# Kernel optimization log

Hardware: AMD Instinct MI355X
Metric: run time of the kernel (lower is better)

## Reference

```python
import jax, jax.numpy as jnp
import numpy as np

# Static config (from set_param of the wrapped deformable conv)
N, CIN, H, W = 8, 64, 128, 128
COUT, KH, KW = 64, 3, 3
STRIDE, PAD, DIL = 1, 1, 1
WEIGHT_BIT = 8
K = KH * KW
HO = (H + 2 * PAD - DIL * (KH - 1) - 1) // STRIDE + 1
WO = (W + 2 * PAD - DIL * (KW - 1) - 1) // STRIDE + 1


def setup_inputs() -> dict:
    key = jax.random.key(0)
    k1, k2, k3 = jax.random.split(key, 3)
    x = jax.random.normal(k1, (N, CIN, H, W), dtype=jnp.float32)
    offset = jax.random.normal(k2, (N, 2 * K, HO, WO), dtype=jnp.float32)
    weight = jax.random.normal(k3, (COUT, CIN, KH, KW), dtype=jnp.float32) * 0.05
    return {"x": x, "offset": offset, "weight": weight}


def quantize_weight_symmetric(w, bits):
    # HAWQ/CoDeNet symmetric per-tensor quant: scale = max(|min|,|max|)/n,
    # q = clamp(round(w/scale), -n-1, n) * scale, straight-through estimator.
    n = 2 ** (bits - 1) - 1
    sat = jnp.maximum(jnp.abs(w.min()), jnp.abs(w.max()))
    scale = jnp.maximum(sat, 1e-8) / n
    wq = jnp.clip(jnp.round(w / scale), -n - 1, n) * scale
    return w + jax.lax.stop_gradient(wq - w)


def deform_conv2d(x, offset, weight):
    # x: [N,C,H,W]; offset: [N, 2*K, HO, WO] (y,x interleaved per kernel tap)
    # Base sampling grid for each kernel tap and output location.
    ky, kx = jnp.meshgrid(jnp.arange(KH), jnp.arange(KW), indexing='ij')
    ky = ky.reshape(K).astype(jnp.float32)  # [K]
    kx = kx.reshape(K).astype(jnp.float32)
    ho = jnp.arange(HO, dtype=jnp.float32)
    wo = jnp.arange(WO, dtype=jnp.float32)
    base_y = ho[None, :, None] * STRIDE - PAD + ky[:, None, None] * DIL  # [K,HO,1]
    base_x = wo[None, None, :] * STRIDE - PAD + kx[:, None, None] * DIL  # [K,1,WO]

    off = offset.reshape(N, K, 2, HO, WO)
    py = base_y[None] + off[:, :, 0]  # [N,K,HO,WO]
    px = base_x[None] + off[:, :, 1]

    y0 = jnp.floor(py)
    x0 = jnp.floor(px)
    dy = py - y0
    dx = px - x0
    y0i = y0.astype(jnp.int32)
    x0i = x0.astype(jnp.int32)

    xf = x.reshape(N, CIN, H * W)

    def gather_corner(yi, xi, wgt):
        # zero padding outside the image
        valid = (yi >= 0) & (yi < H) & (xi >= 0) & (xi < W)
        idx = jnp.clip(yi, 0, H - 1) * W + jnp.clip(xi, 0, W - 1)  # [N,K,HO,WO]
        vals = jax.vmap(lambda xn, idn: xn[:, idn.reshape(-1)])(xf, idx)
        vals = vals.reshape(N, CIN, K, HO, WO)
        return vals * (wgt * valid.astype(wgt.dtype))[:, None]  # [N,1,K,HO,WO]

    sampled = (
        gather_corner(y0i, x0i, (1.0 - dy) * (1.0 - dx))
        + gather_corner(y0i, x0i + 1, (1.0 - dy) * dx)
        + gather_corner(y0i + 1, x0i, dy * (1.0 - dx))
        + gather_corner(y0i + 1, x0i + 1, dy * dx)
    )  # [N,CIN,K,HO,WO]

    out = jnp.einsum('nckhw,ock->nohw', sampled, weight.reshape(COUT, CIN, K))
    return out


def reference(x, offset, weight):
    wq = quantize_weight_symmetric(weight, WEIGHT_BIT)
    return deform_conv2d(x, offset, wq)
```

## Files before the change

kernel.cpp:

```cpp
#include <hip/hip_runtime.h>
#include <hip/hip_bf16.h>

#define NB    8
#define CCH   64
#define HH    128
#define WW    128
#define KTAP  9
#define HW    (HH * WW)
#define KDIM  (CCH * KTAP)
#define KSTEPS 18
#define LDA   72

typedef __attribute__((ext_vector_type(8))) short bf16x8;
typedef __attribute__((ext_vector_type(4))) float f32x4;

__device__ inline unsigned int pack_bf16(float a, float b) {
    unsigned int ua = __float_as_uint(a);
    unsigned int ub = __float_as_uint(b);
    ua += 0x7fffu + ((ua >> 16) & 1u);
    ub += 0x7fffu + ((ub >> 16) & 1u);
    return (ua >> 16) | (ub & 0xffff0000u);
}

__device__ inline void cvt8(uint4 u, float* f) {
    f[0] = __uint_as_float(u.x << 16); f[1] = __uint_as_float(u.x & 0xffff0000u);
    f[2] = __uint_as_float(u.y << 16); f[3] = __uint_as_float(u.y & 0xffff0000u);
    f[4] = __uint_as_float(u.z << 16); f[5] = __uint_as_float(u.z & 0xffff0000u);
    f[6] = __uint_as_float(u.w << 16); f[7] = __uint_as_float(u.w & 0xffff0000u);
}

__global__ __launch_bounds__(256) void maxabs_kernel(const float* __restrict__ w,
                                                     unsigned int* __restrict__ out) {
    unsigned int m = 0;
    int i = blockIdx.x * 1024 + threadIdx.x;
    #pragma unroll
    for (int r = 0; r < 4; r++) {
        m = max(m, __float_as_uint(w[i]) & 0x7fffffffu);
        i += 256;
    }
    #pragma unroll
    for (int off = 32; off > 0; off >>= 1)
        m = max(m, (unsigned int)__shfl_down(m, off));
    if ((threadIdx.x & 63) == 0) atomicMax(out, m);
}

__global__ __launch_bounds__(256) void quant_frag_kernel(const float* __restrict__ w,
                                                         const unsigned int* __restrict__ maxabs_u,
                                                         uint4* __restrict__ bq) {
    int t = blockIdx.x * 256 + threadIdx.x;
    if (t >= 4608) return;
    float m = __uint_as_float(maxabs_u[0]);
    float scale = fmaxf(m, 1e-8f) / 127.f;
    int nt  = t / (KSTEPS * 64);
    int rem = t - nt * (KSTEPS * 64);
    int s    = rem >> 6;
    int lane = rem & 63;
    int quad = lane >> 4, n16 = lane & 15;
    int o = nt * 16 + n16;
    unsigned int u[4];
    #pragma unroll
    for (int jj = 0; jj < 4; jj++) {
        float q[2];
        #pragma unroll
        for (int h = 0; h < 2; h++) {
            int k   = s * 32 + quad * 8 + 2 * jj + h;
            int c   = k & 63;
            int tap = k >> 6;
            float v  = w[(o * CCH + c) * KTAP + tap];
            float qq = rintf(v / scale);
            q[h] = fminf(fmaxf(qq, -128.f), 127.f) * scale;
        }
        u[jj] = pack_bf16(q[0], q[1]);
    }
    bq[t] = make_uint4(u[0], u[1], u[2], u[3]);
}

__global__ __launch_bounds__(256) void transpose_kernel(const float* __restrict__ x,
                                                        unsigned int* __restrict__ xt32) {
    __shared__ float tile[64][65];
    const int t = threadIdx.x;
    const int n = blockIdx.x >> 8;
    const int pbase = (blockIdx.x & 255) * 64;
    #pragma unroll
    for (int i = 0; i < 16; i++) {
        int idx = i * 256 + t;
        int c = idx >> 6, pp = idx & 63;
        tile[c][pp] = x[((size_t)(n * CCH + c)) * HW + pbase + pp];
    }
    __syncthreads();
    #pragma unroll
    for (int j = 0; j < 8; j++) {
        int idx = j * 256 + t;
        int pp = idx >> 5, cp = idx & 31;
        xt32[((size_t)(n * HW + pbase + pp)) * 32 + cp] =
            pack_bf16(tile[2 * cp][pp], tile[2 * cp + 1][pp]);
    }
}

__global__ __launch_bounds__(256) void deform_mfma(const unsigned short* __restrict__ xt,
                                                   const float* __restrict__ offset,
                                                   const uint4* __restrict__ bq,
                                                   float* __restrict__ out) {
    __shared__ unsigned short Abuf[2][64 * LDA];

    const int t    = threadIdx.x;
    const int wid  = t >> 6;
    const int lane = t & 63;
    const int quad = lane >> 4, n16 = lane & 15;
    const int bid  = blockIdx.x;
    const int n    = bid & 7;
    const int px0  = (bid >> 3) * 64;
    const int p_local = t >> 2;
    const int cq      = (t & 3) * 16;
    const int ppx = px0 + p_local;
    const int ho  = ppx >> 7, wo = ppx & 127;

    const unsigned short* xtn = xt + (size_t)n * HW * CCH;
    const float* offn = offset + (size_t)n * 2 * KTAP * HW;

    uint4 bfrag[KSTEPS];
    #pragma unroll
    for (int s = 0; s < KSTEPS; s++)
        bfrag[s] = bq[(wid * KSTEPS + s) * 64 + lane];

    f32x4 acc[4];
    #pragma unroll
    for (int mt = 0; mt < 4; mt++) acc[mt] = (f32x4){0.f, 0.f, 0.f, 0.f};

    auto build = [&](int tap, int buf) {
        const int ky = tap / 3;
        const int kx = tap - 3 * ky;
        const float offy = offn[(2 * tap) * HW + ppx];
        const float offx = offn[(2 * tap + 1) * HW + ppx];
        const float py  = (float)(ho - 1 + ky) + offy;
        const float pxf = (float)(wo - 1 + kx) + offx;
        const float fy = floorf(py), fx = floorf(pxf);
        const int y0 = (int)fy, x0 = (int)fx;
        const float dy = py - fy, dx = pxf - fx;
        const int y1 = y0 + 1, x1 = x0 + 1;
        const bool vy0 = (y0 >= 0) && (y0 < HH);
        const bool vy1 = (y1 >= 0) && (y1 < HH);
        const bool vx0 = (x0 >= 0) && (x0 < WW);
        const bool vx1 = (x1 >= 0) && (x1 < WW);
        const int y0c = min(max(y0, 0), HH - 1);
        const int y1c = min(max(y1, 0), HH - 1);
        const int x0c = min(max(x0, 0), WW - 1);
        const int x1c = min(max(x1, 0), WW - 1);
        const float w00 = (1.f - dy) * (1.f - dx) * ((vy0 && vx0) ? 1.f : 0.f);
        const float w01 = (1.f - dy) * dx         * ((vy0 && vx1) ? 1.f : 0.f);
        const float w10 = dy * (1.f - dx)         * ((vy1 && vx0) ? 1.f : 0.f);
        const float w11 = dy * dx                 * ((vy1 && vx1) ? 1.f : 0.f);

        const unsigned short* p00 = xtn + (y0c * WW + x0c) * CCH + cq;
        const unsigned short* p01 = xtn + (y0c * WW + x1c) * CCH + cq;
        const unsigned short* p10 = xtn + (y1c * WW + x0c) * CCH + cq;
        const unsigned short* p11 = xtn + (y1c * WW + x1c) * CCH + cq;
        uint4 a00 = *(const uint4*)p00, b00 = *(const uint4*)(p00 + 8);
        uint4 a01 = *(const uint4*)p01, b01 = *(const uint4*)(p01 + 8);
        uint4 a10 = *(const uint4*)p10, b10 = *(const uint4*)(p10 + 8);
        uint4 a11 = *(const uint4*)p11, b11 = *(const uint4*)(p11 + 8);

        float s[16], f[16];
        cvt8(a00, f); cvt8(b00, f + 8);
        #pragma unroll
        for (int i = 0; i < 16; i++) s[i] = f[i] * w00;
        cvt8(a01, f); cvt8(b01, f + 8);
        #pragma unroll
        for (int i = 0; i < 16; i++) s[i] = fmaf(f[i], w01, s[i]);
        cvt8(a10, f); cvt8(b10, f + 8);
        #pragma unroll
        for (int i = 0; i < 16; i++) s[i] = fmaf(f[i], w10, s[i]);
        cvt8(a11, f); cvt8(b11, f + 8);
        #pragma unroll
        for (int i = 0; i < 16; i++) s[i] = fmaf(f[i], w11, s[i]);

        unsigned int o8[8];
        #pragma unroll
        for (int i = 0; i < 8; i++) o8[i] = pack_bf16(s[2 * i], s[2 * i + 1]);
        unsigned short* dst = &Abuf[buf][p_local * LDA + cq];
        *(uint4*)dst       = make_uint4(o8[0], o8[1], o8[2], o8[3]);
        *(uint4*)(dst + 8) = make_uint4(o8[4], o8[5], o8[6], o8[7]);
    };

    auto mma_tap = [&](int tap, int buf) {
        #pragma unroll
        for (int sl = 0; sl < 2; sl++) {
            const int sg = tap * 2 + sl;
            bf16x8 b = *(bf16x8*)&bfrag[sg];
            #pragma unroll
            for (int mt = 0; mt < 4; mt++) {
                const unsigned short* src =
                    &Abuf[buf][(mt * 16 + n16) * LDA + sl * 32 + quad * 8];
                bf16x8 a = *(const bf16x8*)src;
                acc[mt] = __builtin_amdgcn_mfma_f32_16x16x32_bf16(a, b, acc[mt], 0, 0, 0);
            }
        }
    };

    build(0, 0);
    __syncthreads();
    for (int tap = 0; tap < KTAP; tap++) {
        if (tap < KTAP - 1) build(tap + 1, (tap + 1) & 1);
        mma_tap(tap, tap & 1);
        __syncthreads();
    }

    const int o = wid * 16 + n16;
    #pragma unroll
    for (int mt = 0; mt < 4; mt++) {
        float4 v = make_float4(acc[mt].x, acc[mt].y, acc[mt].z, acc[mt].w);
        float* dst = out + ((size_t)(n * CCH + o)) * HW + px0 + mt * 16 + quad * 4;
        *(float4*)dst = v;
    }
}

extern "C" void kernel_launch(void* const* d_in, const int* in_sizes, int n_in,
                              void* d_out, int out_size, void* d_ws, size_t ws_size,
                              hipStream_t stream) {
    const float* x      = (const float*)d_in[0];
    const float* offset = (const float*)d_in[1];
    const float* weight = (const float*)d_in[2];
    float* out = (float*)d_out;

    unsigned char* ws = (unsigned char*)d_ws;
    unsigned int* maxabs_u = (unsigned int*)ws;
    uint4*        bq       = (uint4*)(ws + 1024);
    unsigned int* xt32     = (unsigned int*)(ws + 131072);
    unsigned short* xt     = (unsigned short*)xt32;

    hipMemsetAsync(maxabs_u, 0, 4, stream);
    maxabs_kernel<<<36, 256, 0, stream>>>(weight, maxabs_u);
    quant_frag_kernel<<<18, 256, 0, stream>>>(weight, maxabs_u, bq);
    transpose_kernel<<<NB * (HW / 64), 256, 0, stream>>>(x, xt32);
    deform_mfma<<<NB * (HW / 64), 256, 0, stream>>>(xt, offset, bq, out);
}
```

Baseline: 145.3 us.

## Fuse prep kernels, switch to fp16 packed math, precompute sampling indices in LDS

Merges the weight max-abs, quantize and transpose steps into a single prep kernel, which removes the memset and two extra launches. The main kernel now works in fp16 instead of bf16: bilinear interpolation uses packed half-precision vector math and the tensor op is the fp16 MFMA. Each block first computes all per-tap sampling offsets and weights into shared memory. The A tile uses an XOR swizzle instead of padding to avoid LDS bank conflicts. fp16 accumulation of the interpolation lowers precision and could overflow for large inputs.

```diff
diff --git a/kernel.cpp b/kernel.cpp
--- a/kernel.cpp
+++ b/kernel.cpp
@@ -7,93 +7,86 @@
 #define WW    128
 #define KTAP  9
 #define HW    (HH * WW)
-#define KDIM  (CCH * KTAP)
 #define KSTEPS 18
-#define LDA   72
-
-typedef __attribute__((ext_vector_type(8))) short bf16x8;
+
+typedef _Float16 f16x8 __attribute__((ext_vector_type(8)));
+typedef _Float16 f16x2 __attribute__((ext_vector_type(2)));
 typedef __attribute__((ext_vector_type(4))) float f32x4;
 
-__device__ inline unsigned int pack_bf16(float a, float b) {
-    unsigned int ua = __float_as_uint(a);
-    unsigned int ub = __float_as_uint(b);
-    ua += 0x7fffu + ((ua >> 16) & 1u);
-    ub += 0x7fffu + ((ub >> 16) & 1u);
-    return (ua >> 16) | (ub & 0xffff0000u);
-}
-
-__device__ inline void cvt8(uint4 u, float* f) {
-    f[0] = __uint_as_float(u.x << 16); f[1] = __uint_as_float(u.x & 0xffff0000u);
-    f[2] = __uint_as_float(u.y << 16); f[3] = __uint_as_float(u.y & 0xffff0000u);
-    f[4] = __uint_as_float(u.z << 16); f[5] = __uint_as_float(u.z & 0xffff0000u);
-    f[6] = __uint_as_float(u.w << 16); f[7] = __uint_as_float(u.w & 0xffff0000u);
-}
-
-__global__ __launch_bounds__(256) void maxabs_kernel(const float* __restrict__ w,
-                                                     unsigned int* __restrict__ out) {
-    unsigned int m = 0;
-    int i = blockIdx.x * 1024 + threadIdx.x;
-    #pragma unroll
-    for (int r = 0; r < 4; r++) {
-        m = max(m, __float_as_uint(w[i]) & 0x7fffffffu);
-        i += 256;
-    }
-    #pragma unroll
-    for (int off = 32; off > 0; off >>= 1)
-        m = max(m, (unsigned int)__shfl_down(m, off));
-    if ((threadIdx.x & 63) == 0) atomicMax(out, m);
-}
-
-__global__ __launch_bounds__(256) void quant_frag_kernel(const float* __restrict__ w,
-                                                         const unsigned int* __restrict__ maxabs_u,
-                                                         uint4* __restrict__ bq) {
-    int t = blockIdx.x * 256 + threadIdx.x;
-    if (t >= 4608) return;
-    float m = __uint_as_float(maxabs_u[0]);
-    float scale = fmaxf(m, 1e-8f) / 127.f;
-    int nt  = t / (KSTEPS * 64);
-    int rem = t - nt * (KSTEPS * 64);
-    int s    = rem >> 6;
-    int lane = rem & 63;
-    int quad = lane >> 4, n16 = lane & 15;
-    int o = nt * 16 + n16;
-    unsigned int u[4];
-    #pragma unroll
-    for (int jj = 0; jj < 4; jj++) {
-        float q[2];
-        #pragma unroll
-        for (int h = 0; h < 2; h++) {
-            int k   = s * 32 + quad * 8 + 2 * jj + h;
-            int c   = k & 63;
-            int tap = k >> 6;
-            float v  = w[(o * CCH + c) * KTAP + tap];
-            float qq = rintf(v / scale);
-            q[h] = fminf(fmaxf(qq, -128.f), 127.f) * scale;
+__device__ inline unsigned int pack_f16(float a, float b) {
+    f16x2 h;
+    h[0] = (_Float16)a;
+    h[1] = (_Float16)b;
+    return __builtin_bit_cast(unsigned int, h);
+}
+
+__global__ __launch_bounds__(256) void prep_kernel(const float* __restrict__ x,
+                                                   const float* __restrict__ w,
+                                                   unsigned int* __restrict__ xt32,
+                                                   uint4* __restrict__ bq) {
+    __shared__ float tile[64 * 65];
+    const int t = threadIdx.x;
+    const int bid = blockIdx.x;
+
+    if (bid < 2048) {
+        const int n = bid >> 8;
+        const int pbase = (bid & 255) * 64;
+        #pragma unroll
+        for (int i = 0; i < 4; i++) {
+            int idx = i * 256 + t;
+            int c = idx >> 4, f4 = idx & 15;
+            float4 v = *(const float4*)&x[((size_t)(n * CCH + c)) * HW + pbase + f4 * 4];
+            float* d = &tile[c * 65 + f4 * 4];
+            d[0] = v.x; d[1] = v.y; d[2] = v.z; d[3] = v.w;
         }
-        u[jj] = pack_bf16(q[0], q[1]);
-    }
-    bq[t] = make_uint4(u[0], u[1], u[2], u[3]);
-}
-
-__global__ __launch_bounds__(256) void transpose_kernel(const float* __restrict__ x,
-                                                        unsigned int* __restrict__ xt32) {
-    __shared__ float tile[64][65];
-    const int t = threadIdx.x;
-    const int n = blockIdx.x >> 8;
-    const int pbase = (blockIdx.x & 255) * 64;
-    #pragma unroll
-    for (int i = 0; i < 16; i++) {
-        int idx = i * 256 + t;
-        int c = idx >> 6, pp = idx & 63;
-        tile[c][pp] = x[((size_t)(n * CCH + c)) * HW + pbase + pp];
-    }
-    __syncthreads();
-    #pragma unroll
-    for (int j = 0; j < 8; j++) {
-        int idx = j * 256 + t;
-        int pp = idx >> 5, cp = idx & 31;
-        xt32[((size_t)(n * HW + pbase + pp)) * 32 + cp] =
-            pack_bf16(tile[2 * cp][pp], tile[2 * cp + 1][pp]);
+        __syncthreads();
+        const int px = t >> 2, c4 = t & 3;
+        float f[16];
+        #pragma unroll
+        for (int j = 0; j < 16; j++) f[j] = tile[(c4 * 16 + j) * 65 + px];
+        unsigned int o8[8];
+        #pragma unroll
+        for (int i = 0; i < 8; i++) o8[i] = pack_f16(f[2 * i], f[2 * i + 1]);
+        uint4* dst = (uint4*)&xt32[((size_t)(n * HW + pbase + px)) * 32 + c4 * 8];
+        dst[0] = make_uint4(o8[0], o8[1], o8[2], o8[3]);
+        dst[1] = make_uint4(o8[4], o8[5], o8[6], o8[7]);
+    } else {
+        float m = 0.f;
+        for (int i = t; i < CCH * CCH * KTAP; i += 256)
+            m = fmaxf(m, fabsf(w[i]));
+        #pragma unroll
+        for (int off = 32; off > 0; off >>= 1)
+            m = fmaxf(m, __shfl_down(m, off));
+        if ((t & 63) == 0) tile[t >> 6] = m;
+        __syncthreads();
+        m = fmaxf(fmaxf(tile[0], tile[1]), fmaxf(tile[2], tile[3]));
+        const float scale = fmaxf(m, 1e-8f) / 127.f;
+        const float inv_scale = 1.f / scale;
+
+        for (int rec = t; rec < 4608; rec += 256) {
+            int nt  = rec / (KSTEPS * 64);
+            int rem = rec - nt * (KSTEPS * 64);
+            int s    = rem >> 6;
+            int lane = rem & 63;
+            int quad = lane >> 4, n16 = lane & 15;
+            int o = nt * 16 + n16;
+            unsigned int u[4];
+            #pragma unroll
+            for (int jj = 0; jj < 4; jj++) {
+                float q[2];
+                #pragma unroll
+                for (int h = 0; h < 2; h++) {
+                    int k   = s * 32 + quad * 8 + 2 * jj + h;
+                    int c   = k & 63;
+                    int tap = k >> 6;
+                    float v  = w[(o * CCH + c) * KTAP + tap];
+                    float qq = rintf(v * inv_scale);
+                    q[h] = fminf(fmaxf(qq, -128.f), 127.f) * scale;
+                }
+                u[jj] = pack_f16(q[0], q[1]);
+            }
+            bq[rec] = make_uint4(u[0], u[1], u[2], u[3]);
+        }
     }
 }
 
@@ -101,7 +94,9 @@
                                                    const float* __restrict__ offset,
                                                    const uint4* __restrict__ bq,
                                                    float* __restrict__ out) {
-    __shared__ unsigned short Abuf[2][64 * LDA];
+    __shared__ uint4 SIdx[576];
+    __shared__ uint2 SW[576];
+    __shared__ _Float16 Abuf[2][64 * 64];
 
     const int t    = threadIdx.x;
     const int wid  = t >> 6;
@@ -110,12 +105,10 @@
     const int bid  = blockIdx.x;
     const int n    = bid & 7;
     const int px0  = (bid >> 3) * 64;
-    const int p_local = t >> 2;
-    const int cq      = (t & 3) * 16;
-    const int ppx = px0 + p_local;
-    const int ho  = ppx >> 7, wo = ppx & 127;
-
-    const unsigned short* xtn = xt + (size_t)n * HW * CCH;
+    const int pl   = t >> 2;
+    const int c4   = t & 3;
+
+    const char* xb = (const char*)(xt + (size_t)n * HW * CCH);
     const float* offn = offset + (size_t)n * 2 * KTAP * HW;
 
     uint4 bfrag[KSTEPS];
@@ -123,17 +116,13 @@
     for (int s = 0; s < KSTEPS; s++)
         bfrag[s] = bq[(wid * KSTEPS + s) * 64 + lane];
 
-    f32x4 acc[4];
-    #pragma unroll
-    for (int mt = 0; mt < 4; mt++) acc[mt] = (f32x4){0.f, 0.f, 0.f, 0.f};
-
-    auto build = [&](int tap, int buf) {
-        const int ky = tap / 3;
-        const int kx = tap - 3 * ky;
-        const float offy = offn[(2 * tap) * HW + ppx];
-        const float offx = offn[(2 * tap + 1) * HW + ppx];
-        const float py  = (float)(ho - 1 + ky) + offy;
-        const float pxf = (float)(wo - 1 + kx) + offx;
+    for (int u = t; u < 576; u += 256) {
+        const int tap = u >> 6, p = u & 63;
+        const int ppx = px0 + p;
+        const int ho = ppx >> 7, wo = ppx & 127;
+        const int ky = tap / 3, kx = tap - 3 * ky;
+        const float py  = (float)(ho - 1 + ky) + offn[(2 * tap) * HW + ppx];
+        const float pxf = (float)(wo - 1 + kx) + offn[(2 * tap + 1) * HW + ppx];
         const float fy = floorf(py), fx = floorf(pxf);
         const int y0 = (int)fy, x0 = (int)fx;
         const float dy = py - fy, dx = pxf - fx;
@@ -150,53 +139,60 @@
         const float w01 = (1.f - dy) * dx         * ((vy0 && vx1) ? 1.f : 0.f);
         const float w10 = dy * (1.f - dx)         * ((vy1 && vx0) ? 1.f : 0.f);
         const float w11 = dy * dx                 * ((vy1 && vx1) ? 1.f : 0.f);
-
-        const unsigned short* p00 = xtn + (y0c * WW + x0c) * CCH + cq;
-        const unsigned short* p01 = xtn + (y0c * WW + x1c) * CCH + cq;
-        const unsigned short* p10 = xtn + (y1c * WW + x0c) * CCH + cq;
-        const unsigned short* p11 = xtn + (y1c * WW + x1c) * CCH + cq;
-        uint4 a00 = *(const uint4*)p00, b00 = *(const uint4*)(p00 + 8);
-        uint4 a01 = *(const uint4*)p01, b01 = *(const uint4*)(p01 + 8);
-        uint4 a10 = *(const uint4*)p10, b10 = *(const uint4*)(p10 + 8);
-        uint4 a11 = *(const uint4*)p11, b11 = *(const uint4*)(p11 + 8);
-
-        float s[16], f[16];
-        cvt8(a00, f); cvt8(b00, f + 8);
-        #pragma unroll
-        for (int i = 0; i < 16; i++) s[i] = f[i] * w00;
-        cvt8(a01, f); cvt8(b01, f + 8);
-        #pragma unroll
-        for (int i = 0; i < 16; i++) s[i] = fmaf(f[i], w01, s[i]);
-        cvt8(a10, f); cvt8(b10, f + 8);
-        #pragma unroll
-        for (int i = 0; i < 16; i++) s[i] = fmaf(f[i], w10, s[i]);
-        cvt8(a11, f); cvt8(b11, f + 8);
-        #pragma unroll
-        for (int i = 0; i < 16; i++) s[i] = fmaf(f[i], w11, s[i]);
-
-        unsigned int o8[8];
-        #pragma unroll
-        for (int i = 0; i < 8; i++) o8[i] = pack_bf16(s[2 * i], s[2 * i + 1]);
-        unsigned short* dst = &Abuf[buf][p_local * LDA + cq];
-        *(uint4*)dst       = make_uint4(o8[0], o8[1], o8[2], o8[3]);
-        *(uint4*)(dst + 8) = make_uint4(o8[4], o8[5], o8[6], o8[7]);
+        SIdx[u] = make_uint4((unsigned)((y0c * WW + x0c) * 128),
+                             (unsigned)((y0c * WW + x1c) * 128),
+                             (unsigned)((y1c * WW + x0c) * 128),
+                             (unsigned)((y1c * WW + x1c) * 128));
+        SW[u] = make_uint2(pack_f16(w00, w01), pack_f16(w10, w11));
+    }
+
+    f32x4 acc[4];
+    #pragma unroll
+    for (int mt = 0; mt < 4; mt++) acc[mt] = (f32x4){0.f, 0.f, 0.f, 0.f};
+
+    const int cb = c4 * 16;
+    const int p7 = pl & 7;
+
+    auto build = [&](int tap, int buf) {
+        const uint4 ii = SIdx[tap * 64 + pl];
+        const uint2 ww = SW[tap * 64 + pl];
+        const f16x2 wA = __builtin_bit_cast(f16x2, ww.x);
+        const f16x2 wB = __builtin_bit_cast(f16x2, ww.y);
+        const f16x8 a00 = *(const f16x8*)(xb + ii.x + cb);
+        const f16x8 b00 = *(const f16x8*)(xb + ii.x + cb + 64);
+        const f16x8 a01 = *(const f16x8*)(xb + ii.y + cb);
+        const f16x8 b01 = *(const f16x8*)(xb + ii.y + cb + 64);
+        const f16x8 a10 = *(const f16x8*)(xb + ii.z + cb);
+        const f16x8 b10 = *(const f16x8*)(xb + ii.z + cb + 64);
+        const f16x8 a11 = *(const f16x8*)(xb + ii.w + cb);
+        const f16x8 b11 = *(const f16x8*)(xb + ii.w + cb + 64);
+        f16x8 sa = a00 * wA[0];
+        sa += a01 * wA[1];
+        sa += a10 * wB[0];
+        sa += a11 * wB[1];
+        f16x8 sb = b00 * wA[0];
+        sb += b01 * wA[1];
+        sb += b10 * wB[0];
+        sb += b11 * wB[1];
+        *(f16x8*)&Abuf[buf][pl * 64 + ((c4 ^ p7) * 8)]       = sa;
+        *(f16x8*)&Abuf[buf][pl * 64 + (((4 + c4) ^ p7) * 8)] = sb;
     };
 
     auto mma_tap = [&](int tap, int buf) {
         #pragma unroll
         for (int sl = 0; sl < 2; sl++) {
-            const int sg = tap * 2 + sl;
-            bf16x8 b = *(bf16x8*)&bfrag[sg];
+            const f16x8 b = __builtin_bit_cast(f16x8, bfrag[tap * 2 + sl]);
             #pragma unroll
             for (int mt = 0; mt < 4; mt++) {
-                const unsigned short* src =
-                    &Abuf[buf][(mt * 16 + n16) * LDA + sl * 32 + quad * 8];
-                bf16x8 a = *(const bf16x8*)src;
-                acc[mt] = __builtin_amdgcn_mfma_f32_16x16x32_bf16(a, b, acc[mt], 0, 0, 0);
+                const int r = mt * 16 + n16;
+                const int slot = (sl * 4 + quad) ^ (n16 & 7);
+                const f16x8 a = *(const f16x8*)&Abuf[buf][r * 64 + slot * 8];
+                acc[mt] = __builtin_amdgcn_mfma_f32_16x16x32_f16(a, b, acc[mt], 0, 0, 0);
             }
         }
     };
 
+    __syncthreads();
     build(0, 0);
     __syncthreads();
     for (int tap = 0; tap < KTAP; tap++) {
@@ -223,14 +219,10 @@
     float* out = (float*)d_out;
 
     unsigned char* ws = (unsigned char*)d_ws;
-    unsigned int* maxabs_u = (unsigned int*)ws;
-    uint4*        bq       = (uint4*)(ws + 1024);
-    unsigned int* xt32     = (unsigned int*)(ws + 131072);
-    unsigned short* xt     = (unsigned short*)xt32;
-
-    hipMemsetAsync(maxabs_u, 0, 4, stream);
-    maxabs_kernel<<<36, 256, 0, stream>>>(weight, maxabs_u);
-    quant_frag_kernel<<<18, 256, 0, stream>>>(weight, maxabs_u, bq);
-    transpose_kernel<<<NB * (HW / 64), 256, 0, stream>>>(x, xt32);
-    deform_mfma<<<NB * (HW / 64), 256, 0, stream>>>(xt, offset, bq, out);
-}
+    uint4*        bq   = (uint4*)ws;
+    unsigned int* xt32 = (unsigned int*)(ws + 131072);
+    const unsigned short* xt = (const unsigned short*)xt32;
+
+    prep_kernel<<<2049, 256, 0, stream>>>(x, weight, xt32, bq);
+    deform_mfma<<<2048, 256, 0, stream>>>(xt, offset, bq, out);
+}
```

After: 161.7 us. +11.3%, slower.
